# Performance work log

Hardware: AMD Instinct MI355X
Metric: run time of the kernel (lower is better)

Reference implementation:

```python
import jax, jax.numpy as jnp
import numpy as np

B, D = 65536, 512
EPS = 1e-15
MAXN = 1.0 - 4e-3  # geoopt fp32 ball boundary, c = 1


def _norm(x):
    return jnp.sqrt(jnp.clip(jnp.sum(x * x, -1, keepdims=True), EPS))


def _artanh(x):
    return jnp.arctanh(jnp.clip(x, -1.0 + 1e-7, 1.0 - 1e-7))


def projx(x):
    n = _norm(x)
    return jnp.where(n > MAXN, x / n * MAXN, x)


def mobius_add(x, y):
    x2 = jnp.sum(x * x, -1, keepdims=True)
    y2 = jnp.sum(y * y, -1, keepdims=True)
    xy = jnp.sum(x * y, -1, keepdims=True)
    num = (1.0 + 2.0 * xy + y2) * x + (1.0 - x2) * y
    den = 1.0 + 2.0 * xy + x2 * y2
    return num / jnp.maximum(den, EPS)


def expmap(x, u):
    un = _norm(u)
    lam = 2.0 / jnp.maximum(1.0 - jnp.sum(x * x, -1, keepdims=True), EPS)
    return mobius_add(x, jnp.tanh(lam * un / 2.0) * u / un)


def logmap(x, y):
    sub = mobius_add(-x, y)
    sn = _norm(sub)
    lam = 2.0 / jnp.maximum(1.0 - jnp.sum(x * x, -1, keepdims=True), EPS)
    return (2.0 / lam) * _artanh(sn) * sub / sn


def expmap0(u):
    un = _norm(u)
    return jnp.tanh(un) * u / un


def logmap0(y):
    yn = _norm(y)
    return _artanh(yn) * y / yn


def mobius_scalar_mul(r, x):
    xn = _norm(x)
    return jnp.tanh(r * _artanh(xn)) * x / xn


def poincare_fc(x, z, bias):
    # HNN++ Poincare fully-connected layer, c = 1
    zn = jnp.sqrt(jnp.clip(jnp.sum(z * z, 0), EPS))   # [out]
    z_unit = z / zn                                   # [in, out]
    two_r = 2.0 * bias                                # [out]
    cx2 = jnp.sum(x * x, -1, keepdims=True)           # [B, 1]
    inner = x @ z_unit                                # [B, out]
    v = 2.0 * zn * jnp.arcsinh(
        (2.0 * inner * jnp.cosh(two_r) - (1.0 + cx2) * jnp.sinh(two_r))
        / jnp.maximum(1.0 - cx2, EPS))
    w = jnp.sinh(v)
    return w / (1.0 + jnp.sqrt(1.0 + jnp.sum(w * w, -1, keepdims=True)))


def setup_inputs():
    key = jax.random.key(0)
    k1, k2, k3 = jax.random.split(key, 3)
    u1 = jax.random.normal(k1, (B, D), jnp.float32)
    u2 = jax.random.normal(k2, (B, D), jnp.float32)
    # points strictly inside the unit Poincare ball
    x_current = 0.7 * u1 / (1.0 + _norm(u1))
    x_previous = 0.7 * u2 / (1.0 + _norm(u2))
    # PoincareLinear id_init: 0.5*I, plus tiny noise so grads/outputs are non-degenerate
    z = 0.5 * jnp.eye(D, dtype=jnp.float32) + 0.01 * jax.random.normal(k3, (D, D), jnp.float32)
    bias = jnp.zeros((D,), jnp.float32)
    alpha = jnp.asarray(0.7, jnp.float32)
    step_size = jnp.asarray(1.0, jnp.float32)
    return {"x_current": x_current, "x_previous": x_previous, "z": z,
            "bias": bias, "alpha": alpha, "step_size": step_size}


def reference(x_current, x_previous, z, bias, alpha, step_size):
    # backward trajectory via logmap on the manifold (x_previous given)
    bt = logmap(x_previous, x_current)
    step = jax.nn.sigmoid(step_size)
    # PoincareLinear: expmap0 -> poincare_fc -> logmap0
    vel = logmap0(poincare_fc(expmap0(bt), z, bias))
    x_update = projx(expmap(x_current, step * vel))
    a = jax.nn.sigmoid(alpha)
    # poincare_residual_update
    xc = projx(x_current)
    xu = projx(x_update)
    x_next = projx(mobius_add(mobius_scalar_mul(a, xc), mobius_scalar_mul(1.0 - a, xu)))
    return (x_next, xc)
```

## Files before the change

### kernel.cpp

```cpp
#include <hip/hip_runtime.h>
#include <stdint.h>

#define DDIM 512
#define BROWS 65536
#define EPSF 1e-15f
#define MAXNF 0.996f
#define SQRT_EPSF 3.1622776e-8f
#define ATANH_CLIP 0.99999988f

typedef __bf16 bf16x8 __attribute__((ext_vector_type(8)));
typedef float f32x4 __attribute__((ext_vector_type(4)));

__device__ __forceinline__ unsigned short f2bf(float f) {
    union { float f; uint32_t u; } c; c.f = f;
    uint32_t u = c.u;
    u += 0x7fffu + ((u >> 16) & 1u);
    return (unsigned short)(u >> 16);
}

__device__ __forceinline__ float rcpf(float x) { return __builtin_amdgcn_rcpf(x); }

__device__ __forceinline__ float wred(float v) {
    v += __shfl_xor(v, 1);
    v += __shfl_xor(v, 2);
    v += __shfl_xor(v, 4);
    v += __shfl_xor(v, 8);
    v += __shfl_xor(v, 16);
    v += __shfl_xor(v, 32);
    return v;
}

__device__ __forceinline__ float fast_tanh_pos(float x) {
    float t = __expf(-2.0f * x);
    return (1.0f - t) * rcpf(1.0f + t);
}
__device__ __forceinline__ float fast_atanh_pos(float x) {
    return 0.5f * __logf((1.0f + x) * rcpf(1.0f - x));
}
__device__ __forceinline__ float fast_asinh(float t) {
    float a = fabsf(t);
    float r = __logf(a + sqrtf(fmaf(a, a, 1.0f)));
    return copysignf(r, t);
}
__device__ __forceinline__ float fast_sinh(float v) {
    float q = __expf(v);
    return 0.5f * (q - rcpf(q));
}

__global__ void prep_kernel(const float* __restrict__ z, const float* __restrict__ bias,
                            float* __restrict__ znf, float* __restrict__ chv,
                            float* __restrict__ shv, unsigned short* __restrict__ zT) {
    int j = blockIdx.x;
    int l = threadIdx.x;
    float zv[8];
    float s = 0.f;
#pragma unroll
    for (int t = 0; t < 8; ++t) {
        float v = z[(size_t)(t * 64 + l) * DDIM + j];
        zv[t] = v;
        s = fmaf(v, v, s);
    }
    s = wred(s);
    float zn = sqrtf(fmaxf(s, EPSF));
    float inv = 1.0f / zn;
#pragma unroll
    for (int t = 0; t < 8; ++t)
        zT[(size_t)j * DDIM + t * 64 + l] = f2bf(zv[t] * inv);
    if (l == 0) {
        znf[j] = zn;
        float tr = 2.0f * bias[j];
        chv[j] = coshf(tr);
        shv[j] = sinhf(tr);
    }
}

__global__ __launch_bounds__(512, 4) void hpd_main(
    const float* __restrict__ Xc, const float* __restrict__ Xp,
    const float* __restrict__ znf, const float* __restrict__ chv, const float* __restrict__ shv,
    const unsigned short* __restrict__ zT,
    const float* __restrict__ alpha_p, const float* __restrict__ step_p,
    float* __restrict__ out)
{
    __shared__ __align__(16) unsigned char smem[70656];
    float* cx2s = (float*)(smem + 65536);
    float* dccs = (float*)(smem + 65792);
    float* swp  = (float*)(smem + 66048);
    float* cwp  = (float*)(smem + 68096);
    float* ans  = (float*)(smem + 70144);
    float* bns  = (float*)(smem + 70400);

    const int t = threadIdx.x;
    const int w = t >> 6;
    const int l = t & 63;
    const int l15 = l & 15;
    const int quad = l >> 4;
    const int r0 = blockIdx.x * 64;

    float a_sig = rcpf(1.0f + __expf(-alpha_p[0]));
    float step_sig = rcpf(1.0f + __expf(-step_p[0]));

    float* out1 = out + (size_t)BROWS * DDIM;

#pragma unroll
    for (int g = 0; g < 2; ++g) {
        const int rowb = w * 4 + (g << 5);
        float xcv[4][8], xpv[4][8];
#pragma unroll
        for (int q = 0; q < 4; ++q) {
            const float* pc = Xc + (size_t)(r0 + rowb + q) * DDIM + l * 8;
            const float* pp = Xp + (size_t)(r0 + rowb + q) * DDIM + l * 8;
            *(float4*)&xcv[q][0] = *(const float4*)pc;
            *(float4*)&xcv[q][4] = *(const float4*)(pc + 4);
            *(float4*)&xpv[q][0] = *(const float4*)pp;
            *(float4*)&xpv[q][4] = *(const float4*)(pp + 4);
        }
        float dcc[4], dpp[4], dpc[4];
#pragma unroll
        for (int q = 0; q < 4; ++q) {
            float a = 0.f, b = 0.f, c = 0.f;
#pragma unroll
            for (int j = 0; j < 8; ++j) {
                a = fmaf(xcv[q][j], xcv[q][j], a);
                b = fmaf(xpv[q][j], xpv[q][j], b);
                c = fmaf(xpv[q][j], xcv[q][j], c);
            }
            dcc[q] = a; dpp[q] = b; dpc[q] = c;
        }
#pragma unroll
        for (int s = 1; s < 64; s <<= 1) {
#pragma unroll
            for (int q = 0; q < 4; ++q) {
                dcc[q] += __shfl_xor(dcc[q], s);
                dpp[q] += __shfl_xor(dpp[q], s);
                dpc[q] += __shfl_xor(dpc[q], s);
            }
        }
#pragma unroll
        for (int q = 0; q < 4; ++q) {
            const int row = rowb + q;
            float Ca = -(1.0f - 2.0f * dpc[q] + dcc[q]);
            float Cb = 1.0f - dpp[q];
            float den = fmaxf(1.0f - 2.0f * dpc[q] + dpp[q] * dcc[q], EPSF);
            float rden = rcpf(den);
            float ssub = (Ca * Ca * dpp[q] + 2.0f * Ca * Cb * dpc[q] + Cb * Cb * dcc[q]) * rden * rden;
            float sn = sqrtf(fmaxf(ssub, EPSF));
            float tol = fmaxf(1.0f - dpp[q], EPSF);
            float art = fast_atanh_pos(fminf(sn, ATANH_CLIP));
            float sbt = tol * art * rcpf(sn);
            float un = fmaxf(tol * art, SQRT_EPSF);
            float te = fast_tanh_pos(un);
            float se = te * rcpf(un) * sbt;
            float cep = se * Ca * rden;
            float cex = se * Cb * rden;
            if (l == 0) { cx2s[row] = te * te; dccs[row] = dcc[q]; }
            float nx = sqrtf(fmaxf(dcc[q], EPSF));
            float sxc = (nx > MAXNF) ? (MAXNF * rcpf(nx)) : 1.0f;
            float* po1 = out1 + (size_t)(r0 + row) * DDIM + l * 8;
            *(float4*)po1 = make_float4(sxc * xcv[q][0], sxc * xcv[q][1], sxc * xcv[q][2], sxc * xcv[q][3]);
            *(float4*)(po1 + 4) = make_float4(sxc * xcv[q][4], sxc * xcv[q][5], sxc * xcv[q][6], sxc * xcv[q][7]);
            unsigned short e8[8];
#pragma unroll
            for (int j = 0; j < 8; ++j)
                e8[j] = f2bf(fmaf(cex, xcv[q][j], cep * xpv[q][j]));
            uint32_t u0 = (uint32_t)e8[0] | ((uint32_t)e8[1] << 16);
            uint32_t u1 = (uint32_t)e8[2] | ((uint32_t)e8[3] << 16);
            uint32_t u2 = (uint32_t)e8[4] | ((uint32_t)e8[5] << 16);
            uint32_t u3 = (uint32_t)e8[6] | ((uint32_t)e8[7] << 16);
            uint32_t off = row * 1024 + ((l ^ (row & 7)) * 16);
            *(uint4*)(smem + off) = make_uint4(u0, u1, u2, u3);
        }
    }
    __syncthreads();

    f32x4 acc[4][4];
#pragma unroll
    for (int m = 0; m < 4; ++m)
#pragma unroll
        for (int j = 0; j < 4; ++j)
            acc[m][j] = (f32x4){0.f, 0.f, 0.f, 0.f};

    const unsigned short* zbase = zT + (size_t)(w * 64 + l15) * DDIM + quad * 8;
    bf16x8 bbuf[2][4];
#pragma unroll
    for (int j = 0; j < 4; ++j)
        bbuf[0][j] = *(const bf16x8*)(zbase + (size_t)j * 16 * DDIM);
#pragma unroll
    for (int ks = 0; ks < 16; ++ks) {
        const int cur = ks & 1;
        if (ks < 15) {
#pragma unroll
            for (int j = 0; j < 4; ++j)
                bbuf[cur ^ 1][j] = *(const bf16x8*)(zbase + (size_t)j * 16 * DDIM + (ks + 1) * 32);
        }
        bf16x8 af[4];
#pragma unroll
        for (int m = 0; m < 4; ++m) {
            int row = m * 16 + l15;
            af[m] = *(const bf16x8*)(smem + row * 1024 + (((ks * 4 + quad) ^ (row & 7)) * 16));
        }
#pragma unroll
        for (int m = 0; m < 4; ++m)
#pragma unroll
            for (int j = 0; j < 4; ++j)
                acc[m][j] = __builtin_amdgcn_mfma_f32_16x16x32_bf16(af[m], bbuf[cur][j], acc[m][j], 0, 0, 0);
    }

    float znv[4], chc[4], shc[4];
#pragma unroll
    for (int j = 0; j < 4; ++j) {
        int col = w * 64 + j * 16 + l15;
        znv[j] = znf[col]; chc[j] = chv[col]; shc[j] = shv[col];
    }
    const float* xb = Xc + (size_t)r0 * DDIM + w * 64 + l15;

#pragma unroll
    for (int m = 0; m < 4; ++m) {
        int rbase = m * 16 + quad * 4;
        float xv[4][4];
#pragma unroll
        for (int j = 0; j < 4; ++j)
#pragma unroll
            for (int r = 0; r < 4; ++r)
                xv[j][r] = xb[(size_t)(rbase + r) * DDIM + j * 16];
        float inv1m[4], opc[4];
#pragma unroll
        for (int r = 0; r < 4; ++r) {
            float c2 = cx2s[rbase + r];
            inv1m[r] = rcpf(fmaxf(1.0f - c2, EPSF));
            opc[r] = 1.0f + c2;
        }
        float swr[4] = {0.f, 0.f, 0.f, 0.f}, cwr[4] = {0.f, 0.f, 0.f, 0.f};
#pragma unroll
        for (int j = 0; j < 4; ++j) {
#pragma unroll
            for (int r = 0; r < 4; ++r) {
                float inner = acc[m][j][r];
                float arg = fmaf(2.0f * inner, chc[j], -opc[r] * shc[j]) * inv1m[r];
                float v = 2.0f * znv[j] * fast_asinh(arg);
                float wv = fast_sinh(v);
                acc[m][j][r] = wv;
                swr[r] = fmaf(wv, wv, swr[r]);
                cwr[r] = fmaf(xv[j][r], wv, cwr[r]);
            }
        }
#pragma unroll
        for (int r = 0; r < 4; ++r) {
            float s = swr[r], c = cwr[r];
            s += __shfl_xor(s, 1); s += __shfl_xor(s, 2); s += __shfl_xor(s, 4); s += __shfl_xor(s, 8);
            c += __shfl_xor(c, 1); c += __shfl_xor(c, 2); c += __shfl_xor(c, 4); c += __shfl_xor(c, 8);
            if (l15 == 0) { swp[(rbase + r) * 8 + w] = s; cwp[(rbase + r) * 8 + w] = c; }
        }
    }
    __syncthreads();

    if (t < 64) {
        int row = t;
        float4 s0 = *(const float4*)(swp + row * 8);
        float4 s1 = *(const float4*)(swp + row * 8 + 4);
        float sw = ((s0.x + s0.y) + (s0.z + s0.w)) + ((s1.x + s1.y) + (s1.z + s1.w));
        float4 q0 = *(const float4*)(cwp + row * 8);
        float4 q1 = *(const float4*)(cwp + row * 8 + 4);
        float cw = ((q0.x + q0.y) + (q0.z + q0.w)) + ((q1.x + q1.y) + (q1.z + q1.w));
        float dcc = dccs[row];
        float is = 1.0f / (1.0f + sqrtf(1.0f + sw));
        float nfc = sqrtf(fmaxf(sw * is * is, EPSF));
        float artf = fast_atanh_pos(fminf(nfc, ATANH_CLIP));
        float un2 = fmaxf(step_sig * artf, SQRT_EPSF);
        float g = fast_tanh_pos(un2 / fmaxf(1.0f - dcc, EPSF));
        float by = g * is / nfc;
        float xy = by * cw;
        float y2 = by * by * sw;
        float P = 1.0f + 2.0f * xy + y2;
        float den2 = fmaxf(1.0f + 2.0f * xy + dcc * y2, EPSF);
        float a1 = P / den2;
        float b1 = (1.0f - dcc) * by / den2;
        float s2u = a1 * a1 * dcc + 2.0f * a1 * b1 * cw + b1 * b1 * sw;
        float nxu = sqrtf(fmaxf(s2u, EPSF));
        float pj = (nxu > MAXNF) ? (MAXNF / nxu) : 1.0f;
        a1 *= pj; b1 *= pj;
        float nxu2 = fminf(nxu, MAXNF);
        float nx = sqrtf(fmaxf(dcc, EPSF));
        float sxc = (nx > MAXNF) ? (MAXNF / nx) : 1.0f;
        float nxc = fminf(nx, MAXNF);
        float A1 = fast_tanh_pos(a_sig * fast_atanh_pos(fminf(nxc, ATANH_CLIP))) / nxc * sxc;
        float t2s = fast_tanh_pos((1.0f - a_sig) * fast_atanh_pos(fminf(nxu2, ATANH_CLIP)));
        float sm2 = t2s / fmaxf(nxu2, SQRT_EPSF);
        float A2 = sm2 * a1, B2 = sm2 * b1;
        float x2m = A1 * A1 * dcc;
        float y2m = A2 * A2 * dcc + 2.0f * A2 * B2 * cw + B2 * B2 * sw;
        float xym = A1 * (A2 * dcc + B2 * cw);
        float num1 = 1.0f + 2.0f * xym + y2m;
        float num2 = 1.0f - x2m;
        float den3 = fmaxf(1.0f + 2.0f * xym + x2m * y2m, EPSF);
        float an = (num1 * A1 + num2 * A2) / den3;
        float bn = (num2 * B2) / den3;
        float s2n = an * an * dcc + 2.0f * an * bn * cw + bn * bn * sw;
        float nn = sqrtf(fmaxf(s2n, EPSF));
        float pj2 = (nn > MAXNF) ? (MAXNF / nn) : 1.0f;
        ans[row] = an * pj2;
        bns[row] = bn * pj2;
    }
    __syncthreads();

    float* ob = out + (size_t)r0 * DDIM + w * 64 + l15;
#pragma unroll
    for (int m = 0; m < 4; ++m) {
        int rbase = m * 16 + quad * 4;
        float xv[4][4];
#pragma unroll
        for (int j = 0; j < 4; ++j)
#pragma unroll
            for (int r = 0; r < 4; ++r)
                xv[j][r] = xb[(size_t)(rbase + r) * DDIM + j * 16];
        float anv[4], bnv[4];
#pragma unroll
        for (int r = 0; r < 4; ++r) { anv[r] = ans[rbase + r]; bnv[r] = bns[rbase + r]; }
#pragma unroll
        for (int j = 0; j < 4; ++j) {
#pragma unroll
            for (int r = 0; r < 4; ++r)
                ob[(size_t)(rbase + r) * DDIM + j * 16] = fmaf(anv[r], xv[j][r], bnv[r] * acc[m][j][r]);
        }
    }
}

extern "C" void kernel_launch(void* const* d_in, const int* in_sizes, int n_in,
                              void* d_out, int out_size, void* d_ws, size_t ws_size,
                              hipStream_t stream) {
    const float* xc = (const float*)d_in[0];
    const float* xp = (const float*)d_in[1];
    const float* z = (const float*)d_in[2];
    const float* bias = (const float*)d_in[3];
    const float* alpha = (const float*)d_in[4];
    const float* stepsz = (const float*)d_in[5];
    float* out = (float*)d_out;

    float* znf = (float*)d_ws;
    float* chv = znf + 512;
    float* shv = znf + 1024;
    unsigned short* zT = (unsigned short*)(znf + 1536);

    prep_kernel<<<512, 64, 0, stream>>>(z, bias, znf, chv, shv, zT);
    hpd_main<<<BROWS / 64, 512, 0, stream>>>(xc, xp, znf, chv, shv, zT, alpha, stepsz, out);
}
```

Before: 563.1 us.

## Split fused kernel into row-prep phase and GEMM phase via global bf16 staging

Replaces the prep+fused main kernel pair with two kernels. The first computes per-row norms, the logmap/expmap0 operand and projx(x_current), and writes a pre-swizzled bf16 tile to a 64 MB workspace. It also folds the z-normalisation prep into its first 512 blocks. The second kernel streams that tile into LDS with global_load_lds and runs the MFMA GEMM plus the epilogue. The aim is to shorten the long serial prologue of each block and raise overlap. The cost is an extra write and read of the staged operand through HBM, and correctness depends on the out1 pointer offset and on enough workspace being provided.

After: 597.6 us. 1.06x slower.

```diff
diff --git a/kernel.cpp b/kernel.cpp
--- a/kernel.cpp
+++ b/kernel.cpp
@@ -71,6 +71,309 @@
         float tr = 2.0f * bias[j];
         chv[j] = coshf(tr);
         shv[j] = sinhf(tr);
+    }
+}
+
+__global__ __launch_bounds__(512, 4) void hpd_phase_a(
+    const float* __restrict__ Xc, const float* __restrict__ Xp,
+    const float* __restrict__ z, const float* __restrict__ bias,
+    float* __restrict__ out1, unsigned short* __restrict__ e_glob,
+    float* __restrict__ cx2_g, float* __restrict__ dcc_g,
+    float* __restrict__ znf, float* __restrict__ chv, float* __restrict__ shv,
+    unsigned short* __restrict__ zT)
+{
+    const int t = threadIdx.x;
+    const int w = t >> 6;
+    const int l = t & 63;
+    const int r0 = blockIdx.x * 64;
+    unsigned char* etile = (unsigned char*)(e_glob + (size_t)blockIdx.x * 32768);
+
+#pragma unroll
+    for (int g = 0; g < 2; ++g) {
+        const int rowb = w * 4 + (g << 5);
+        float xcv[4][8], xpv[4][8];
+#pragma unroll
+        for (int q = 0; q < 4; ++q) {
+            const float* pc = Xc + (size_t)(r0 + rowb + q) * DDIM + l * 8;
+            const float* pp = Xp + (size_t)(r0 + rowb + q) * DDIM + l * 8;
+            *(float4*)&xcv[q][0] = *(const float4*)pc;
+            *(float4*)&xcv[q][4] = *(const float4*)(pc + 4);
+            *(float4*)&xpv[q][0] = *(const float4*)pp;
+            *(float4*)&xpv[q][4] = *(const float4*)(pp + 4);
+        }
+        float dcc[4], dpp[4], dpc[4];
+#pragma unroll
+        for (int q = 0; q < 4; ++q) {
+            float a = 0.f, b = 0.f, c = 0.f;
+#pragma unroll
+            for (int j = 0; j < 8; ++j) {
+                a = fmaf(xcv[q][j], xcv[q][j], a);
+                b = fmaf(xpv[q][j], xpv[q][j], b);
+                c = fmaf(xpv[q][j], xcv[q][j], c);
+            }
+            dcc[q] = a; dpp[q] = b; dpc[q] = c;
+        }
+#pragma unroll
+        for (int s = 1; s < 64; s <<= 1) {
+#pragma unroll
+            for (int q = 0; q < 4; ++q) {
+                dcc[q] += __shfl_xor(dcc[q], s);
+                dpp[q] += __shfl_xor(dpp[q], s);
+                dpc[q] += __shfl_xor(dpc[q], s);
+            }
+        }
+#pragma unroll
+        for (int q = 0; q < 4; ++q) {
+            const int row = rowb + q;
+            float Ca = -(1.0f - 2.0f * dpc[q] + dcc[q]);
+            float Cb = 1.0f - dpp[q];
+            float den = fmaxf(1.0f - 2.0f * dpc[q] + dpp[q] * dcc[q], EPSF);
+            float rden = rcpf(den);
+            float ssub = (Ca * Ca * dpp[q] + 2.0f * Ca * Cb * dpc[q] + Cb * Cb * dcc[q]) * rden * rden;
+            float sn = sqrtf(fmaxf(ssub, EPSF));
+            float tol = fmaxf(1.0f - dpp[q], EPSF);
+            float art = fast_atanh_pos(fminf(sn, ATANH_CLIP));
+            float sbt = tol * art * rcpf(sn);
+            float un = fmaxf(tol * art, SQRT_EPSF);
+            float te = fast_tanh_pos(un);
+            float se = te * rcpf(un) * sbt;
+            float cep = se * Ca * rden;
+            float cex = se * Cb * rden;
+            if (l == 0) { cx2_g[r0 + row] = te * te; dcc_g[r0 + row] = dcc[q]; }
+            float nx = sqrtf(fmaxf(dcc[q], EPSF));
+            float sxc = (nx > MAXNF) ? (MAXNF * rcpf(nx)) : 1.0f;
+            float* po1 = out1 + (size_t)(r0 + row) * DDIM + l * 8;
+            *(float4*)po1 = make_float4(sxc * xcv[q][0], sxc * xcv[q][1], sxc * xcv[q][2], sxc * xcv[q][3]);
+            *(float4*)(po1 + 4) = make_float4(sxc * xcv[q][4], sxc * xcv[q][5], sxc * xcv[q][6], sxc * xcv[q][7]);
+            unsigned short e8[8];
+#pragma unroll
+            for (int j = 0; j < 8; ++j)
+                e8[j] = f2bf(fmaf(cex, xcv[q][j], cep * xpv[q][j]));
+            uint32_t u0 = (uint32_t)e8[0] | ((uint32_t)e8[1] << 16);
+            uint32_t u1 = (uint32_t)e8[2] | ((uint32_t)e8[3] << 16);
+            uint32_t u2 = (uint32_t)e8[4] | ((uint32_t)e8[5] << 16);
+            uint32_t u3 = (uint32_t)e8[6] | ((uint32_t)e8[7] << 16);
+            uint32_t off = row * 1024 + ((l ^ (row & 7)) * 16);
+            *(uint4*)(etile + off) = make_uint4(u0, u1, u2, u3);
+        }
+    }
+
+    if (blockIdx.x < 512 && t < 64) {
+        const int j = blockIdx.x;
+        float zv[8];
+        float s = 0.f;
+#pragma unroll
+        for (int k = 0; k < 8; ++k) {
+            float v = z[(size_t)(k * 64 + l) * DDIM + j];
+            zv[k] = v;
+            s = fmaf(v, v, s);
+        }
+        s = wred(s);
+        float zn = sqrtf(fmaxf(s, EPSF));
+        float inv = 1.0f / zn;
+#pragma unroll
+        for (int k = 0; k < 8; ++k)
+            zT[(size_t)j * DDIM + k * 64 + l] = f2bf(zv[k] * inv);
+        if (l == 0) {
+            znf[j] = zn;
+            float tr = 2.0f * bias[j];
+            chv[j] = coshf(tr);
+            shv[j] = sinhf(tr);
+        }
+    }
+}
+
+__global__ __launch_bounds__(512, 4) void hpd_gemm(
+    const float* __restrict__ Xc,
+    const float* __restrict__ znf, const float* __restrict__ chv, const float* __restrict__ shv,
+    const unsigned short* __restrict__ zT, const unsigned short* __restrict__ e_glob,
+    const float* __restrict__ cx2_g, const float* __restrict__ dcc_g,
+    const float* __restrict__ alpha_p, const float* __restrict__ step_p,
+    float* __restrict__ out)
+{
+    __shared__ __align__(16) unsigned char smem[70400];
+    float* cx2s = (float*)(smem + 65536);
+    float* swp  = (float*)(smem + 65792);
+    float* cwp  = (float*)(smem + 67840);
+    float* ans  = (float*)(smem + 69888);
+    float* bns  = (float*)(smem + 70144);
+
+    const int t = threadIdx.x;
+    const int w = t >> 6;
+    const int l = t & 63;
+    const int l15 = l & 15;
+    const int quad = l >> 4;
+    const int r0 = blockIdx.x * 64;
+
+    const unsigned char* gsrc = (const unsigned char*)(e_glob + (size_t)blockIdx.x * 32768);
+#pragma unroll
+    for (int i = 0; i < 8; ++i) {
+        const int off = (w * 8 + i) * 1024;
+        __builtin_amdgcn_global_load_lds(
+            (const __attribute__((address_space(1))) void*)(gsrc + off + l * 16),
+            (__attribute__((address_space(3))) void*)(smem + off), 16, 0, 0);
+    }
+    if (w == 0)
+        __builtin_amdgcn_global_load_lds(
+            (const __attribute__((address_space(1))) void*)(cx2_g + r0 + l),
+            (__attribute__((address_space(3))) void*)cx2s, 4, 0, 0);
+
+    float a_sig = rcpf(1.0f + __expf(-alpha_p[0]));
+    float step_sig = rcpf(1.0f + __expf(-step_p[0]));
+
+    float znv[4], chc[4], shc[4];
+#pragma unroll
+    for (int j = 0; j < 4; ++j) {
+        int col = w * 64 + j * 16 + l15;
+        znv[j] = znf[col]; chc[j] = chv[col]; shc[j] = shv[col];
+    }
+
+    f32x4 acc[4][4];
+#pragma unroll
+    for (int m = 0; m < 4; ++m)
+#pragma unroll
+        for (int j = 0; j < 4; ++j)
+            acc[m][j] = (f32x4){0.f, 0.f, 0.f, 0.f};
+
+    const unsigned short* zbase = zT + (size_t)(w * 64 + l15) * DDIM + quad * 8;
+    bf16x8 bbuf[2][4];
+#pragma unroll
+    for (int j = 0; j < 4; ++j)
+        bbuf[0][j] = *(const bf16x8*)(zbase + (size_t)j * 16 * DDIM);
+
+    __syncthreads();
+
+#pragma unroll
+    for (int ks = 0; ks < 16; ++ks) {
+        const int cur = ks & 1;
+        if (ks < 15) {
+#pragma unroll
+            for (int j = 0; j < 4; ++j)
+                bbuf[cur ^ 1][j] = *(const bf16x8*)(zbase + (size_t)j * 16 * DDIM + (ks + 1) * 32);
+        }
+        bf16x8 af[4];
+#pragma unroll
+        for (int m = 0; m < 4; ++m) {
+            int row = m * 16 + l15;
+            af[m] = *(const bf16x8*)(smem + row * 1024 + (((ks * 4 + quad) ^ (row & 7)) * 16));
+        }
+#pragma unroll
+        for (int m = 0; m < 4; ++m)
+#pragma unroll
+            for (int j = 0; j < 4; ++j)
+                acc[m][j] = __builtin_amdgcn_mfma_f32_16x16x32_bf16(af[m], bbuf[cur][j], acc[m][j], 0, 0, 0);
+    }
+
+    const float* xb = Xc + (size_t)r0 * DDIM + w * 64 + l15;
+
+#pragma unroll
+    for (int m = 0; m < 4; ++m) {
+        int rbase = m * 16 + quad * 4;
+        float xv[4][4];
+#pragma unroll
+        for (int j = 0; j < 4; ++j)
+#pragma unroll
+            for (int r = 0; r < 4; ++r)
+                xv[j][r] = xb[(size_t)(rbase + r) * DDIM + j * 16];
+        float inv1m[4], opc[4];
+#pragma unroll
+        for (int r = 0; r < 4; ++r) {
+            float c2 = cx2s[rbase + r];
+            inv1m[r] = rcpf(fmaxf(1.0f - c2, EPSF));
+            opc[r] = 1.0f + c2;
+        }
+        float swr[4] = {0.f, 0.f, 0.f, 0.f}, cwr[4] = {0.f, 0.f, 0.f, 0.f};
+#pragma unroll
+        for (int j = 0; j < 4; ++j) {
+#pragma unroll
+            for (int r = 0; r < 4; ++r) {
+                float inner = acc[m][j][r];
+                float arg = fmaf(2.0f * inner, chc[j], -opc[r] * shc[j]) * inv1m[r];
+                float v = 2.0f * znv[j] * fast_asinh(arg);
+                float wv = fast_sinh(v);
+                acc[m][j][r] = wv;
+                swr[r] = fmaf(wv, wv, swr[r]);
+                cwr[r] = fmaf(xv[j][r], wv, cwr[r]);
+            }
+        }
+#pragma unroll
+        for (int r = 0; r < 4; ++r) {
+            float s = swr[r], c = cwr[r];
+            s += __shfl_xor(s, 1); s += __shfl_xor(s, 2); s += __shfl_xor(s, 4); s += __shfl_xor(s, 8);
+            c += __shfl_xor(c, 1); c += __shfl_xor(c, 2); c += __shfl_xor(c, 4); c += __shfl_xor(c, 8);
+            if (l15 == 0) { swp[(rbase + r) * 8 + w] = s; cwp[(rbase + r) * 8 + w] = c; }
+        }
+    }
+    __syncthreads();
+
+    if (t < 64) {
+        int row = t;
+        float4 s0 = *(const float4*)(swp + row * 8);
+        float4 s1 = *(const float4*)(swp + row * 8 + 4);
+        float sw = ((s0.x + s0.y) + (s0.z + s0.w)) + ((s1.x + s1.y) + (s1.z + s1.w));
+        float4 q0 = *(const float4*)(cwp + row * 8);
+        float4 q1 = *(const float4*)(cwp + row * 8 + 4);
+        float cw = ((q0.x + q0.y) + (q0.z + q0.w)) + ((q1.x + q1.y) + (q1.z + q1.w));
+        float dcc = dcc_g[r0 + row];
+        float is = 1.0f / (1.0f + sqrtf(1.0f + sw));
+        float nfc = sqrtf(fmaxf(sw * is * is, EPSF));
+        float artf = fast_atanh_pos(fminf(nfc, ATANH_CLIP));
+        float un2 = fmaxf(step_sig * artf, SQRT_EPSF);
+        float g = fast_tanh_pos(un2 / fmaxf(1.0f - dcc, EPSF));
+        float by = g * is / nfc;
+        float xy = by * cw;
+        float y2 = by * by * sw;
+        float P = 1.0f + 2.0f * xy + y2;
+        float den2 = fmaxf(1.0f + 2.0f * xy + dcc * y2, EPSF);
+        float a1 = P / den2;
+        float b1 = (1.0f - dcc) * by / den2;
+        float s2u = a1 * a1 * dcc + 2.0f * a1 * b1 * cw + b1 * b1 * sw;
+        float nxu = sqrtf(fmaxf(s2u, EPSF));
+        float pj = (nxu > MAXNF) ? (MAXNF / nxu) : 1.0f;
+        a1 *= pj; b1 *= pj;
+        float nxu2 = fminf(nxu, MAXNF);
+        float nx = sqrtf(fmaxf(dcc, EPSF));
+        float sxc = (nx > MAXNF) ? (MAXNF / nx) : 1.0f;
+        float nxc = fminf(nx, MAXNF);
+        float A1 = fast_tanh_pos(a_sig * fast_atanh_pos(fminf(nxc, ATANH_CLIP))) / nxc * sxc;
+        float t2s = fast_tanh_pos((1.0f - a_sig) * fast_atanh_pos(fminf(nxu2, ATANH_CLIP)));
+        float sm2 = t2s / fmaxf(nxu2, SQRT_EPSF);
+        float A2 = sm2 * a1, B2 = sm2 * b1;
+        float x2m = A1 * A1 * dcc;
+        float y2m = A2 * A2 * dcc + 2.0f * A2 * B2 * cw + B2 * B2 * sw;
+        float xym = A1 * (A2 * dcc + B2 * cw);
+        float num1 = 1.0f + 2.0f * xym + y2m;
+        float num2 = 1.0f - x2m;
+        float den3 = fmaxf(1.0f + 2.0f * xym + x2m * y2m, EPSF);
+        float an = (num1 * A1 + num2 * A2) / den3;
+        float bn = (num2 * B2) / den3;
+        float s2n = an * an * dcc + 2.0f * an * bn * cw + bn * bn * sw;
+        float nn = sqrtf(fmaxf(s2n, EPSF));
+        float pj2 = (nn > MAXNF) ? (MAXNF / nn) : 1.0f;
+        ans[row] = an * pj2;
+        bns[row] = bn * pj2;
+    }
+    __syncthreads();
+
+    float* ob = out + (size_t)r0 * DDIM + w * 64 + l15;
+#pragma unroll
+    for (int m = 0; m < 4; ++m) {
+        int rbase = m * 16 + quad * 4;
+        float xv[4][4];
+#pragma unroll
+        for (int j = 0; j < 4; ++j)
+#pragma unroll
+            for (int r = 0; r < 4; ++r)
+                xv[j][r] = xb[(size_t)(rbase + r) * DDIM + j * 16];
+        float anv[4], bnv[4];
+#pragma unroll
+        for (int r = 0; r < 4; ++r) { anv[r] = ans[rbase + r]; bnv[r] = bns[rbase + r]; }
+#pragma unroll
+        for (int j = 0; j < 4; ++j) {
+#pragma unroll
+            for (int r = 0; r < 4; ++r)
+                ob[(size_t)(rbase + r) * DDIM + j * 16] = fmaf(anv[r], xv[j][r], bnv[r] * acc[m][j][r]);
+        }
     }
 }
 
@@ -334,12 +637,24 @@
     const float* alpha = (const float*)d_in[4];
     const float* stepsz = (const float*)d_in[5];
     float* out = (float*)d_out;
+    float* out1 = out + (size_t)BROWS * DDIM;
 
     float* znf = (float*)d_ws;
     float* chv = znf + 512;
     float* shv = znf + 1024;
     unsigned short* zT = (unsigned short*)(znf + 1536);
 
-    prep_kernel<<<512, 64, 0, stream>>>(z, bias, znf, chv, shv, zT);
-    hpd_main<<<BROWS / 64, 512, 0, stream>>>(xc, xp, znf, chv, shv, zT, alpha, stepsz, out);
-}
+    const size_t NEEDED = 6144 + 524288 + 262144 + 262144 + 67108864;
+    if (ws_size >= NEEDED) {
+        float* cx2_g = (float*)((char*)d_ws + 6144 + 524288);
+        float* dcc_g = cx2_g + 65536;
+        unsigned short* e_glob = (unsigned short*)(dcc_g + 65536);
+        hpd_phase_a<<<BROWS / 64, 512, 0, stream>>>(xc, xp, z, bias, out1, e_glob,
+                                                    cx2_g, dcc_g, znf, chv, shv, zT);
+        hpd_gemm<<<BROWS / 64, 512, 0, stream>>>(xc, znf, chv, shv, zT, e_glob,
+                                                 cx2_g, dcc_g, alpha, stepsz, out);
+    } else {
+        prep_kernel<<<512, 64, 0, stream>>>(z, bias, znf, chv, shv, zT);
+        hpd_main<<<BROWS / 64, 512, 0, stream>>>(xc, xp, znf, chv, shv, zT, alpha, stepsz, out);
+    }
+}
```
